# Kernel optimization log

Measured on AMD Instinct MI355X. Metric: run time of the kernel, lower is better.

## Reference

```python
import jax, jax.numpy as jnp
import numpy as np

B, S, LW = 64, 128, 20
CHAR_V, CHAR_E, CHAR_C = 100, 30, 30
WORD_V, WORD_E = 100000, 300
H, NC = 256, 25
F = WORD_E + CHAR_C  # 330


def setup_inputs() -> dict:
    key = jax.random.key(0)
    ks = jax.random.split(key, 16)
    u = lambda k, shape, s: jax.random.uniform(k, shape, jnp.float32, -s, s)
    sent = jax.random.randint(ks[0], (B, S), 0, WORD_V)
    word = jax.random.randint(ks[1], (B, S, LW), 0, CHAR_V)
    tag = jax.random.randint(ks[2], (B, S), 0, NC)
    lengths = jax.random.randint(ks[3], (B,), S // 2, S + 1)
    mask = jnp.arange(S)[None, :] < lengths[:, None]  # [B,S] bool, mask[:,0] all True

    word_table = u(ks[4], (WORD_V, WORD_E), 0.5)
    char_table = u(ks[5], (CHAR_V, CHAR_E), (3.0 / CHAR_E) ** 0.5)
    conv_w = u(ks[6], (CHAR_C, CHAR_E, 3), (6.0 / (CHAR_E * 3 + CHAR_C)) ** 0.5)
    conv_b = jnp.zeros((CHAR_C,), jnp.float32)

    def lstm_params(k):
        k1, k2 = jax.random.split(k)
        s_ih = (6.0 / (4 * H + F)) ** 0.5
        s_hh = (6.0 / (4 * H + H)) ** 0.5
        w_ih = u(k1, (4 * H, F), s_ih)
        w_hh = u(k2, (4 * H, H), s_hh)
        # b_ih + b_hh, each with forget-gate slice [H:2H] = 1.0 -> combined 2.0
        b = jnp.zeros((4 * H,), jnp.float32).at[H:2 * H].set(2.0)
        return w_ih, w_hh, b

    w_ih_f, w_hh_f, b_f = lstm_params(ks[7])
    w_ih_r, w_hh_r, b_r = lstm_params(ks[8])
    s_lin = (6.0 / (NC + 2 * H)) ** 0.5
    lin_w = u(ks[9], (NC, 2 * H), s_lin)
    lin_b = jnp.zeros((NC,), jnp.float32)
    start_t = u(ks[10], (NC,), 0.1)
    end_t = u(ks[11], (NC,), 0.1)
    trans = u(ks[12], (NC, NC), 0.1)
    return dict(word_table=word_table, char_table=char_table, conv_w=conv_w,
                conv_b=conv_b, w_ih_f=w_ih_f, w_hh_f=w_hh_f, b_f=b_f,
                w_ih_r=w_ih_r, w_hh_r=w_hh_r, b_r=b_r, lin_w=lin_w, lin_b=lin_b,
                start_t=start_t, end_t=end_t, trans=trans,
                sent=sent, word=word, tag=tag, mask=mask)


def _lstm_dir(x, w_ih, w_hh, b, reverse):
    # x: [B,S,F] -> precompute input projections time-major [S,B,4H]
    gx = jnp.einsum('bsf,gf->sbg', x, w_ih) + b
    bsz = x.shape[0]
    hs = w_hh.shape[1]

    def step(carry, g):
        h, c = carry
        g = g + h @ w_hh.T
        i, f, gg, o = jnp.split(g, 4, axis=-1)
        c = jax.nn.sigmoid(f) * c + jax.nn.sigmoid(i) * jnp.tanh(gg)
        h = jax.nn.sigmoid(o) * jnp.tanh(c)
        return (h, c), h

    init = (jnp.zeros((bsz, hs), x.dtype), jnp.zeros((bsz, hs), x.dtype))
    _, hseq = jax.lax.scan(step, init, gx, reverse=reverse)
    return hseq  # [S,B,H]


def _crf_nll(em, tg, mk, start_t, end_t, trans):
    # em: [S,B,C] emissions; tg: [S,B] int; mk: [S,B] float (mk[0]=1)
    bsz = em.shape[1]
    bidx = jnp.arange(bsz)
    # numerator: gold path score
    em_tag = jnp.take_along_axis(em, tg[..., None], axis=-1)[..., 0]   # [S,B]
    tr = trans[tg[:-1], tg[1:]]                                        # [S-1,B]
    score = start_t[tg[0]] + em_tag[0] + jnp.sum(mk[1:] * (tr + em_tag[1:]), axis=0)
    last = mk.sum(0).astype(jnp.int32) - 1
    score = score + end_t[tg[last, bidx]]
    # denominator: forward algorithm (logsumexp scan over time)
    alpha0 = start_t[None, :] + em[0]                                   # [B,C]

    def step(alpha, xs):
        em_t, mk_t = xs
        nxt = jax.nn.logsumexp(alpha[:, :, None] + trans[None, :, :] + em_t[:, None, :], axis=1)
        alpha = jnp.where(mk_t[:, None] > 0, nxt, alpha)
        return alpha, None

    alpha, _ = jax.lax.scan(step, alpha0, (em[1:], mk[1:]))
    logZ = jax.nn.logsumexp(alpha + end_t[None, :], axis=1)
    return -jnp.sum(score - logZ)  # model returns -log_likelihood (reduction='sum')


def reference(word_table, char_table, conv_w, conv_b, w_ih_f, w_hh_f, b_f,
              w_ih_r, w_hh_r, b_r, lin_w, lin_b, start_t, end_t, trans,
              sent, word, tag, mask):
    # --- char CNN encoder (dropout = identity in eval; no ReLU in original forward) ---
    ct = char_table.at[0].set(0.0)                      # padding_idx=0
    cemb = ct[word]                                     # [B,S,LW,E]
    x = cemb.reshape(B * S, LW, CHAR_E).transpose(0, 2, 1)  # [BS,E,LW]
    conv = jax.lax.conv_general_dilated(
        x, conv_w, window_strides=(1,), padding=[(1, 1)],
        dimension_numbers=('NCH', 'OIH', 'NCH')) + conv_b[None, :, None]
    char_feat = conv.max(axis=2).reshape(B, S, CHAR_C)  # global max-pool over chars
    # --- word embedding + concat ---
    wemb = word_table[sent]                             # [B,S,WORD_E]
    feat = jnp.concatenate([wemb, char_feat], axis=2)   # [B,S,F]
    # --- biLSTM ---
    hf = _lstm_dir(feat, w_ih_f, w_hh_f, b_f, reverse=False)
    hr = _lstm_dir(feat, w_ih_r, w_hh_r, b_r, reverse=True)
    h = jnp.concatenate([hf, hr], axis=-1)              # [S,B,2H] time-major
    em = h @ lin_w.T + lin_b                            # [S,B,NC]
    # --- CRF negative log-likelihood ---
    tg = tag.T
    mk = mask.T.astype(em.dtype)
    return _crf_nll(em, tg, mk, start_t, end_t, trans)
```

## Files before the change

### kernel.cpp

```cpp
#include <hip/hip_runtime.h>
#include <math.h>

#define B_  64
#define S_  128
#define LW_ 20
#define CHAR_E_ 30
#define CHAR_C_ 30
#define WORD_E_ 300
#define H_  256
#define NC_ 25
#define F_  330
#define KP_ 352
#define G4_ 1024
#define NG_ 2048

typedef __attribute__((ext_vector_type(8))) short short8;
typedef __attribute__((ext_vector_type(4))) float floatx4;
typedef __attribute__((ext_vector_type(8))) int int8v;

__device__ __forceinline__ unsigned int f2bf(float f){
    unsigned int u = __float_as_uint(f);
    u += 0x7FFFu + ((u>>16)&1u);
    return (u>>16) & 0xFFFFu;
}
__device__ __forceinline__ float bf2f(unsigned int v){ return __uint_as_float(v<<16); }

__device__ __forceinline__ float bfh(uint2 pk, int g){
    unsigned int w = (g < 2) ? pk.x : pk.y;
    return __uint_as_float((g & 1) ? (w & 0xffff0000u) : (w << 16));
}

__device__ __forceinline__ float sigf_(float x){ return __builtin_amdgcn_rcpf(1.0f+__expf(-x)); }
__device__ __forceinline__ float tanhf2_(float x){ return 1.0f - 2.0f*__builtin_amdgcn_rcpf(1.0f+__expf(2.0f*x)); }

__device__ __forceinline__ void gload16(const void* g, void* l){
    __builtin_amdgcn_global_load_lds((const __attribute__((address_space(1))) unsigned int*)g,
                                     (__attribute__((address_space(3))) unsigned int*)l, 16, 0, 0);
}

#define BAR_LDS() __asm__ volatile("s_waitcnt lgkmcnt(0)\n\ts_barrier" ::: "memory")

__global__ __launch_bounds__(256) void k_prep(const float* ct, const int* word,
        const float* cw, const float* cb, const float* wt, const int* sent,
        const float* wf, const float* wr, float* out,
        unsigned short* feat, unsigned short* wpack){
    __shared__ __align__(16) float x[8][32][20];
    int blk = blockIdx.x;
    int tid = threadIdx.x;
    if(blk < 1024){
        int tok0 = blk*8;
        for(int e = tid; e < 8*32*20; e += 256){
            int t  = e % 20;
            int ic = (e/20) & 31;
            int tl = e / 640;
            int id = word[(size_t)(tok0+tl)*LW_ + t];
            float v = 0.f;
            if(ic < CHAR_E_ && id != 0) v = ct[(size_t)id*CHAR_E_ + ic];
            x[tl][ic][t] = v;
        }
        __syncthreads();
        if(tid < 240){
            int tl = tid/30, oc = tid%30;
            float acc[22];
            #pragma unroll
            for(int q=0;q<22;q++) acc[q] = 0.f;
            for(int ic=0; ic<CHAR_E_; ic++){
                float w0 = cw[(oc*CHAR_E_+ic)*3+0];
                float w1 = cw[(oc*CHAR_E_+ic)*3+1];
                float w2 = cw[(oc*CHAR_E_+ic)*3+2];
                const float* xr = &x[tl][ic][0];
                #pragma unroll
                for(int t4=0;t4<5;t4++){
                    float4 v = ((const float4*)xr)[t4];
                    int t0 = t4*4;
                    acc[t0+2] += v.x*w0; acc[t0+1] += v.x*w1; acc[t0+0] += v.x*w2;
                    acc[t0+3] += v.y*w0; acc[t0+2] += v.y*w1; acc[t0+1] += v.y*w2;
                    acc[t0+4] += v.z*w0; acc[t0+3] += v.z*w1; acc[t0+2] += v.z*w2;
                    acc[t0+5] += v.w*w0; acc[t0+4] += v.w*w1; acc[t0+3] += v.w*w2;
                }
            }
            float m = -1e30f;
            #pragma unroll
            for(int t=0;t<20;t++){ float v = acc[t+1]; m = fmaxf(m, v); }
            m += cb[oc];
            feat[(size_t)(tok0+tl)*KP_ + WORD_E_ + oc] = (unsigned short)f2bf(m);
        }
    } else if(blk < 1024+2432){
        int idx = (blk-1024)*256 + tid;
        int n = idx / 76, e4 = idx % 76;
        if(e4 < 75){
            float4 v = ((const float4*)(wt + (size_t)sent[n]*WORD_E_))[e4];
            unsigned int lo = f2bf(v.x) | (f2bf(v.y)<<16);
            unsigned int hi = f2bf(v.z) | (f2bf(v.w)<<16);
            uint2 pr; pr.x = lo; pr.y = hi;
            *(uint2*)(feat + (size_t)n*KP_ + e4*4) = pr;
        } else {
            unsigned int* z = (unsigned int*)(feat + (size_t)n*KP_ + 330);
            #pragma unroll
            for(int q=0;q<11;q++) z[q] = 0;
        }
    } else if(blk < 6272){
        int i = (blk-3456)*256 + tid;
        int r = i / KP_, k = i % KP_;
        const float* src = (r < G4_) ? wf : wr;
        int rr = r & (G4_-1);
        wpack[i] = (k < F_) ? (unsigned short)f2bf(src[(size_t)rr*F_ + k]) : 0;
    } else {
        if(tid == 0) *out = 0.f;
    }
}

__global__ __launch_bounds__(256) void k_gemm(const unsigned short* A, const unsigned short* Bw,
                                              const float* bf, const float* br, unsigned short* gxb){
    __shared__ __align__(16) unsigned short As[128*32];
    __shared__ __align__(16) unsigned short Bs[128*32];
    int m0 = blockIdx.x*128, n0 = blockIdx.y*128;
    int tid = threadIdx.x;
    int w = tid>>6, lane = tid&63, q = lane>>4, l16 = lane&15;
    int wr = w>>1, wc = w&1;
    int srow0 = w*32 + (lane>>2);
    int scol  = (lane&3)*8;
    floatx4 acc[4][4];
    #pragma unroll
    for(int i=0;i<4;i++)
        #pragma unroll
        for(int j=0;j<4;j++) acc[i][j] = (floatx4){0.f,0.f,0.f,0.f};

    for(int k0=0; k0<KP_; k0+=32){
        __syncthreads();
        gload16(A  + (size_t)(m0+srow0   )*KP_ + k0 + scol, (unsigned short*)As + w*1024      );
        gload16(A  + (size_t)(m0+srow0+16)*KP_ + k0 + scol, (unsigned short*)As + w*1024 + 512);
        gload16(Bw + (size_t)(n0+srow0   )*KP_ + k0 + scol, (unsigned short*)Bs + w*1024      );
        gload16(Bw + (size_t)(n0+srow0+16)*KP_ + k0 + scol, (unsigned short*)Bs + w*1024 + 512);
        __asm__ volatile("s_waitcnt vmcnt(0)" ::: "memory");
        __syncthreads();
        short8 a_[4], b_[4];
        #pragma unroll
        for(int i=0;i<4;i++) a_[i] = *(const short8*)&As[(wr*64 + i*16 + l16)*32 + q*8];
        #pragma unroll
        for(int j=0;j<4;j++) b_[j] = *(const short8*)&Bs[(wc*64 + j*16 + l16)*32 + q*8];
        #pragma unroll
        for(int i=0;i<4;i++)
            #pragma unroll
            for(int j=0;j<4;j++)
                acc[i][j] = __builtin_amdgcn_mfma_f32_16x16x32_bf16(a_[i], b_[j], acc[i][j], 0,0,0);
    }
    #pragma unroll
    for(int j=0;j<4;j++){
        int n = n0 + wc*64 + j*16 + l16;
        int dirr = n >> 10, grow = n & 1023;
        float bias = dirr ? br[grow] : bf[grow];
        int gg = grow >> 8;
        int u  = grow & 255;
        int w8 = u >> 5, uu = u & 31;
        #pragma unroll
        for(int i=0;i<4;i++){
            int mb = m0 + wr*64 + i*16 + q*4;
            #pragma unroll
            for(int r=0;r<4;r++){
                int m = mb + r;
                int b = m >> 7, s = m & 127;
                size_t idx = ((size_t)(dirr*128 + s)*32 + (size_t)(b>>1))*2048
                           + (size_t)w8*256 + (size_t)((b&1)*32 + uu)*4 + gg;
                gxb[idx] = (unsigned short)f2bf(acc[i][j][r] + bias);
            }
        }
    }
}

__device__ __forceinline__ void lstm_step2(
    const unsigned char* hbb, unsigned char* hpub,
    float* wl, const int8v (*wreg)[2][2],
    int l16, int q, int bb, int uu,
    uint2 gg, float& cc, float* hs_ptr, const float inv_sc)
{
    floatx4 a[4][2];
    #pragma unroll
    for(int g=0; g<4; g++){
        a[g][0] = (floatx4){0.f,0.f,0.f,0.f};
        a[g][1] = (floatx4){0.f,0.f,0.f,0.f};
    }
    #pragma unroll
    for(int ki=0; ki<2; ki++){
        int8v hb = *(const int8v*)&hbb[l16*272 + ki*128 + q*32];
        #pragma unroll
        for(int g=0; g<4; g++){
            a[g][0] = __builtin_amdgcn_mfma_scale_f32_16x16x128_f8f6f4(wreg[g][0][ki], hb, a[g][0], 0,0,0,0x7F,0,0x7F);
            a[g][1] = __builtin_amdgcn_mfma_scale_f32_16x16x128_f8f6f4(wreg[g][1][ki], hb, a[g][1], 0,0,0,0x7F,0,0x7F);
        }
    }
    if(l16 < 2){
        #pragma unroll
        for(int g=0; g<4; g++){
            *(floatx4*)&wl[g*72 + l16*36 + q*4     ] = a[g][0];
            *(floatx4*)&wl[g*72 + l16*36 + q*4 + 16] = a[g][1];
        }
    }
    float iv = wl[0*72 + bb*36 + uu]*inv_sc + bfh(gg,0);
    float fv = wl[1*72 + bb*36 + uu]*inv_sc + bfh(gg,1);
    float gv = wl[2*72 + bb*36 + uu]*inv_sc + bfh(gg,2);
    float ov = wl[3*72 + bb*36 + uu]*inv_sc + bfh(gg,3);
    float cn = sigf_(fv)*cc + sigf_(iv)*tanhf2_(gv);
    cc = cn;
    float hv = sigf_(ov)*tanhf2_(cn);
    *hs_ptr = hv;
    unsigned int d8 = __builtin_amdgcn_cvt_pk_fp8_f32(hv*16.f, hv*16.f, 0u, false) & 0xFFu;
    unsigned int pk = d8
        | ((unsigned int)__shfl_down((int)d8, 1) << 8)
        | ((unsigned int)__shfl_down((int)d8, 2) << 16)
        | ((unsigned int)__shfl_down((int)d8, 3) << 24);
    if((uu & 3) == 0) *(unsigned int*)hpub = pk;
    BAR_LDS();
}

__global__ __launch_bounds__(512,2) void k_lstm_all(const float* whhf, const float* whhr,
        const unsigned short* gxb, float* hseq)
{
    int bid = blockIdx.x;
    int dir = bid >> 5;
    int bgrp = bid & 31;
    int tid = threadIdx.x;
    int w    = tid >> 6;
    int lane = tid & 63;
    int q    = lane >> 4;
    int l16  = lane & 15;
    int bb   = lane >> 5;
    int uu   = lane & 31;

    __shared__ __align__(16) unsigned char hlds[2][16*272];
    __shared__ __align__(16) float wregion[8*288];

    const float* whh = dir ? whhr : whhf;

    int8v wreg[4][2][2];
    #pragma unroll
    for(int g=0; g<4; g++){
        #pragma unroll
        for(int j=0; j<2; j++){
            const float* rp = whh + (size_t)(g*H_ + w*32 + j*16 + l16)*H_;
            #pragma unroll
            for(int ki=0; ki<2; ki++){
                const float* p = rp + ki*128 + q*32;
                int8v acc;
                #pragma unroll
                for(int wd=0; wd<8; wd++){
                    unsigned int d = 0;
                    d = __builtin_amdgcn_cvt_pk_fp8_f32(p[wd*4+0]*64.f, p[wd*4+1]*64.f, d, false);
                    d = __builtin_amdgcn_cvt_pk_fp8_f32(p[wd*4+2]*64.f, p[wd*4+3]*64.f, d, true);
                    acc[wd] = (int)d;
                }
                wreg[g][j][ki] = acc;
            }
        }
    }

    for(int i = tid; i < 2*16*272/4; i += 512) ((unsigned int*)hlds)[i] = 0;
    __syncthreads();

    const float inv_sc = 1.0f/1024.f;
    float cc = 0.f;

    int s0 = dir ? (S_-1) : 0;
    long gstep = dir ? -65536 : 65536;
    const unsigned short* gp = gxb + (size_t)(dir*128 + s0)*65536 + (size_t)bgrp*2048 + w*256 + lane*4;
    long hstep = dir ? -(long)(B_*H_) : (long)(B_*H_);
    float* hp = hseq + (((size_t)dir*S_ + s0)*B_ + bgrp*2 + bb)*H_ + w*32 + uu;

    float* wl = &wregion[w*288];
    unsigned char* hpw0 = &hlds[0][bb*272 + w*32 + (uu & ~3)];
    unsigned char* hpw1 = &hlds[1][bb*272 + w*32 + (uu & ~3)];

    uint2 P = *(const uint2*)gp; gp += gstep;
    uint2 Q;

    for(int t=0; t<S_; t+=2){
        Q = *(const uint2*)gp; gp += gstep;
        lstm_step2(&hlds[0][0], hpw1, wl, wreg, l16, q, bb, uu, P, cc, hp, inv_sc);
        hp += hstep;
        P = *(const uint2*)gp; gp += gstep;
        lstm_step2(&hlds[1][0], hpw0, wl, wreg, l16, q, bb, uu, Q, cc, hp, inv_sc);
        hp += hstep;
    }
}

__global__ __launch_bounds__(256) void k_em(const float* hseq, const float* lw, const float* lb, float* em){
    __shared__ __align__(16) float hb[8][516];
    int sb0 = blockIdx.x*8;
    int tid = threadIdx.x;
    for(int i = tid; i < 1024; i += 256){
        int p = i >> 7, r = i & 127;
        int sb = sb0 + p, s = sb >> 6, b = sb & 63;
        const float* src = (r < 64) ? (hseq + (((size_t)0*S_+s)*B_+b)*H_ + r*4)
                                    : (hseq + (((size_t)1*S_+s)*B_+b)*H_ + (r-64)*4);
        *(float4*)&hb[p][r*4] = *(const float4*)src;
    }
    __syncthreads();
    if(tid < 200){
        int p = tid / 25, nc = tid % 25;
        const float4* wv = (const float4*)(lw + (size_t)nc*2*H_);
        const float4* hv = (const float4*)&hb[p][0];
        float acc = lb[nc];
        #pragma unroll 16
        for(int k=0;k<128;k++){ float4 a=hv[k], ww=wv[k]; acc += a.x*ww.x + a.y*ww.y + a.z*ww.z + a.w*ww.w; }
        em[(size_t)(sb0+p)*NC_ + nc] = acc;
    }
}

__global__ void k_crf(const float* em, const int* tag, const void* mask,
                      const float* st, const float* et, const float* tr, float* out){
    __shared__ float trs[NC_*NC_];
    int b = blockIdx.x, tid = threadIdx.x;
    for(int i=tid;i<NC_*NC_;i+=64) trs[i]=tr[i];
    unsigned int first = *(const unsigned int*)mask;
    int ml;
    if(first == 1u) ml = 0;
    else if(first == 0x3F800000u) ml = 2;
    else ml = 1;
    __syncthreads();

    float part = 0.f; int cnt = 0;
    for(int s = tid; s < S_; s += 64){
        float mkv;
        {
            int off = b*S_ + s;
            if(ml==0)      mkv = ((const int*)mask)[off] ? 1.f : 0.f;
            else if(ml==1) mkv = ((const unsigned char*)mask)[off] ? 1.f : 0.f;
            else           mkv = ((const float*)mask)[off];
        }
        cnt += (mkv != 0.f) ? 1 : 0;
        if(s == 0){
            int t0 = tag[b*S_];
            part += st[t0] + em[((size_t)0*B_ + b)*NC_ + t0];
        } else {
            int tp = tag[b*S_ + s-1], tc = tag[b*S_ + s];
            part += mkv * (trs[tp*NC_ + tc] + em[((size_t)s*B_ + b)*NC_ + tc]);
        }
    }
    for(int o=32;o>0;o>>=1){ part += __shfl_down(part, o); cnt += __shfl_down(cnt, o); }
    float score = 0.f;
    int len = __shfl(cnt, 0);
    float score0 = __shfl(part, 0);
    if(tid == 0) score = score0 + et[ tag[b*S_ + len-1] ];

    float Ecol[NC_];
    if(tid < NC_){
        #pragma unroll
        for(int i=0;i<NC_;i++) Ecol[i] = __expf(trs[i*NC_+tid]);
    } else {
        #pragma unroll
        for(int i=0;i<NC_;i++) Ecol[i] = 0.f;
    }

    float alpha = (tid < NC_) ? (st[tid] + em[((size_t)0*B_ + b)*NC_ + tid]) : -1e30f;
    float em_n = (tid < NC_) ? em[((size_t)1*B_ + b)*NC_ + tid] : 0.f;

    for(int s=1;s<S_;s++){
        float em_c = em_n;
        if(s+1 < S_) em_n = (tid < NC_) ? em[((size_t)(s+1)*B_ + b)*NC_ + tid] : 0.f;
        float mkv;
        {
            int off = b*S_ + s;
            if(ml==0)      mkv = ((const int*)mask)[off] ? 1.f : 0.f;
            else if(ml==1) mkv = ((const unsigned char*)mask)[off] ? 1.f : 0.f;
            else           mkv = ((const float*)mask)[off];
        }
        float v = alpha;
        #pragma unroll
        for(int o=16;o>0;o>>=1) v = fmaxf(v, __shfl_down(v, o));
        float m = __shfl(v, 0);
        float a = (tid < NC_) ? __expf(alpha - m) : 0.f;
        float S0 = 0.f, S1 = 0.f;
        #pragma unroll
        for(int i=0;i<24;i+=2){ S0 += __shfl(a, i) * Ecol[i]; S1 += __shfl(a, i+1) * Ecol[i+1]; }
        S0 += __shfl(a, 24) * Ecol[24];
        float nxt = m + __logf(S0 + S1) + em_c;
        if(tid < NC_ && mkv != 0.f) alpha = nxt;
    }

    float v = (tid < NC_) ? (alpha + et[tid]) : -1e30f;
    float m2 = v;
    #pragma unroll
    for(int o=16;o>0;o>>=1) m2 = fmaxf(m2, __shfl_down(m2, o));
    m2 = __shfl(m2, 0);
    float e = (tid < NC_) ? __expf(v - m2) : 0.f;
    #pragma unroll
    for(int o=16;o>0;o>>=1) e += __shfl_down(e, o);
    if(tid == 0){
        float logZ = m2 + __logf(e);
        atomicAdd(out, logZ - score);
    }
}

extern "C" void kernel_launch(void* const* d_in, const int* in_sizes, int n_in,
                              void* d_out, int out_size, void* d_ws, size_t ws_size,
                              hipStream_t stream) {
    const float* word_table = (const float*)d_in[0];
    const float* char_table = (const float*)d_in[1];
    const float* conv_w     = (const float*)d_in[2];
    const float* conv_b     = (const float*)d_in[3];
    const float* w_ih_f     = (const float*)d_in[4];
    const float* w_hh_f     = (const float*)d_in[5];
    const float* b_f        = (const float*)d_in[6];
    const float* w_ih_r     = (const float*)d_in[7];
    const float* w_hh_r     = (const float*)d_in[8];
    const float* b_r        = (const float*)d_in[9];
    const float* lin_w      = (const float*)d_in[10];
    const float* lin_b      = (const float*)d_in[11];
    const float* start_t    = (const float*)d_in[12];
    const float* end_t      = (const float*)d_in[13];
    const float* trans      = (const float*)d_in[14];
    const int*   sent       = (const int*)d_in[15];
    const int*   word       = (const int*)d_in[16];
    const int*   tag        = (const int*)d_in[17];
    const void*  mask       = d_in[18];
    float* out = (float*)d_out;

    char* ws = (char*)d_ws;
    unsigned short* feat  = (unsigned short*)ws;
    unsigned short* wpack = (unsigned short*)(ws + 5767168);
    unsigned short* gxb   = (unsigned short*)(ws + 5767168 + 1441792);
    float* hseq = (float*)(ws + 5767168 + 1441792 + 33554432);
    float* em   = (float*)(ws + 5767168 + 1441792 + 33554432 + 16777216);

    k_prep<<<dim3(6273), 256, 0, stream>>>(char_table, word, conv_w, conv_b,
                                           word_table, sent, w_ih_f, w_ih_r, out, feat, wpack);
    k_gemm<<<dim3(B_*S_/128, NG_/128), 256, 0, stream>>>(feat, wpack, b_f, b_r, gxb);
    k_lstm_all<<<dim3(64), 512, 0, stream>>>(w_hh_f, w_hh_r, gxb, hseq);
    k_em<<<dim3(S_*B_/8), 256, 0, stream>>>(hseq, lin_w, lin_b, em);
    k_crf<<<dim3(B_), 64, 0, stream>>>(em, tag, mask, start_t, end_t, trans, out);
}
```

Before: 580.6 us.

## Split LSTM recurrence across 16 wavefronts of 16 hidden units each

The recurrent LSTM kernel now runs 1024 threads per block, with 16 wavefronts each owning 16 hidden units instead of 8 wavefronts owning 32. Each wave issues half as many MFMAs per step and stores the fp8 hidden byte directly, with no shuffle packing. The GEMM output layout for the gate pre-activations is changed to match the new per-wave slicing. The aim is a shorter serial per-step critical path. In exchange, only half the lanes do the elementwise gate math, and the per-step barrier now covers more waves.

```diff
diff --git a/kernel.cpp b/kernel.cpp
--- a/kernel.cpp
+++ b/kernel.cpp
@@ -150,9 +150,10 @@
         int n = n0 + wc*64 + j*16 + l16;
         int dirr = n >> 10, grow = n & 1023;
         float bias = dirr ? br[grow] : bf[grow];
-        int gg = grow >> 8;
-        int u  = grow & 255;
-        int w8 = u >> 5, uu = u & 31;
+        int gg  = grow >> 8;
+        int ug  = grow & 255;
+        int w16 = ug >> 4, u = ug & 15;
+        int ubase = w16*128 + u*4 + gg;
         #pragma unroll
         for(int i=0;i<4;i++){
             int mb = m0 + wr*64 + i*16 + q*4;
@@ -160,125 +161,113 @@
             for(int r=0;r<4;r++){
                 int m = mb + r;
                 int b = m >> 7, s = m & 127;
-                size_t idx = ((size_t)(dirr*128 + s)*32 + (size_t)(b>>1))*2048
-                           + (size_t)w8*256 + (size_t)((b&1)*32 + uu)*4 + gg;
+                size_t idx = ((size_t)((dirr*128 + s)*32 + (b>>1)))*2048
+                           + (size_t)(ubase + (b&1)*64);
                 gxb[idx] = (unsigned short)f2bf(acc[i][j][r] + bias);
             }
         }
     }
 }
 
-__device__ __forceinline__ void lstm_step2(
+__device__ __forceinline__ void lstm_step16w(
     const unsigned char* hbb, unsigned char* hpub,
-    float* wl, const int8v (*wreg)[2][2],
-    int l16, int q, int bb, int uu,
+    float* wl, const int8v (*wreg)[2],
+    int l16, int q, int lane,
     uint2 gg, float& cc, float* hs_ptr, const float inv_sc)
 {
-    floatx4 a[4][2];
-    #pragma unroll
-    for(int g=0; g<4; g++){
-        a[g][0] = (floatx4){0.f,0.f,0.f,0.f};
-        a[g][1] = (floatx4){0.f,0.f,0.f,0.f};
-    }
+    floatx4 a[4];
+    #pragma unroll
+    for(int g=0; g<4; g++) a[g] = (floatx4){0.f,0.f,0.f,0.f};
     #pragma unroll
     for(int ki=0; ki<2; ki++){
         int8v hb = *(const int8v*)&hbb[l16*272 + ki*128 + q*32];
         #pragma unroll
-        for(int g=0; g<4; g++){
-            a[g][0] = __builtin_amdgcn_mfma_scale_f32_16x16x128_f8f6f4(wreg[g][0][ki], hb, a[g][0], 0,0,0,0x7F,0,0x7F);
-            a[g][1] = __builtin_amdgcn_mfma_scale_f32_16x16x128_f8f6f4(wreg[g][1][ki], hb, a[g][1], 0,0,0,0x7F,0,0x7F);
-        }
+        for(int g=0; g<4; g++)
+            a[g] = __builtin_amdgcn_mfma_scale_f32_16x16x128_f8f6f4(wreg[g][ki], hb, a[g], 0,0,0,0x7F,0,0x7F);
     }
     if(l16 < 2){
         #pragma unroll
-        for(int g=0; g<4; g++){
-            *(floatx4*)&wl[g*72 + l16*36 + q*4     ] = a[g][0];
-            *(floatx4*)&wl[g*72 + l16*36 + q*4 + 16] = a[g][1];
-        }
-    }
-    float iv = wl[0*72 + bb*36 + uu]*inv_sc + bfh(gg,0);
-    float fv = wl[1*72 + bb*36 + uu]*inv_sc + bfh(gg,1);
-    float gv = wl[2*72 + bb*36 + uu]*inv_sc + bfh(gg,2);
-    float ov = wl[3*72 + bb*36 + uu]*inv_sc + bfh(gg,3);
-    float cn = sigf_(fv)*cc + sigf_(iv)*tanhf2_(gv);
-    cc = cn;
-    float hv = sigf_(ov)*tanhf2_(cn);
-    *hs_ptr = hv;
-    unsigned int d8 = __builtin_amdgcn_cvt_pk_fp8_f32(hv*16.f, hv*16.f, 0u, false) & 0xFFu;
-    unsigned int pk = d8
-        | ((unsigned int)__shfl_down((int)d8, 1) << 8)
-        | ((unsigned int)__shfl_down((int)d8, 2) << 16)
-        | ((unsigned int)__shfl_down((int)d8, 3) << 24);
-    if((uu & 3) == 0) *(unsigned int*)hpub = pk;
+        for(int g=0; g<4; g++)
+            *(floatx4*)&wl[g*32 + l16*16 + q*4] = a[g];
+    }
+    if(lane < 32){
+        float iv = wl[0*32 + lane]*inv_sc + bfh(gg,0);
+        float fv = wl[1*32 + lane]*inv_sc + bfh(gg,1);
+        float gv = wl[2*32 + lane]*inv_sc + bfh(gg,2);
+        float ov = wl[3*32 + lane]*inv_sc + bfh(gg,3);
+        float cn = sigf_(fv)*cc + sigf_(iv)*tanhf2_(gv);
+        cc = cn;
+        float hv = sigf_(ov)*tanhf2_(cn);
+        *hs_ptr = hv;
+        unsigned int d8 = __builtin_amdgcn_cvt_pk_fp8_f32(hv*16.f, hv*16.f, 0u, false) & 0xFFu;
+        *hpub = (unsigned char)d8;
+    }
     BAR_LDS();
 }
 
-__global__ __launch_bounds__(512,2) void k_lstm_all(const float* whhf, const float* whhr,
+__global__ __launch_bounds__(1024,4) void k_lstm_all(const float* whhf, const float* whhr,
         const unsigned short* gxb, float* hseq)
 {
     int bid = blockIdx.x;
     int dir = bid >> 5;
     int bgrp = bid & 31;
     int tid = threadIdx.x;
-    int w    = tid >> 6;
+    int w16  = tid >> 6;
     int lane = tid & 63;
     int q    = lane >> 4;
     int l16  = lane & 15;
-    int bb   = lane >> 5;
-    int uu   = lane & 31;
+    int bb   = lane >> 4;
+    int u    = lane & 15;
 
     __shared__ __align__(16) unsigned char hlds[2][16*272];
-    __shared__ __align__(16) float wregion[8*288];
+    __shared__ __align__(16) float wregion[16*128];
 
     const float* whh = dir ? whhr : whhf;
 
-    int8v wreg[4][2][2];
+    int8v wreg[4][2];
     #pragma unroll
     for(int g=0; g<4; g++){
-        #pragma unroll
-        for(int j=0; j<2; j++){
-            const float* rp = whh + (size_t)(g*H_ + w*32 + j*16 + l16)*H_;
-            #pragma unroll
-            for(int ki=0; ki<2; ki++){
-                const float* p = rp + ki*128 + q*32;
-                int8v acc;
-                #pragma unroll
-                for(int wd=0; wd<8; wd++){
-                    unsigned int d = 0;
-                    d = __builtin_amdgcn_cvt_pk_fp8_f32(p[wd*4+0]*64.f, p[wd*4+1]*64.f, d, false);
-                    d = __builtin_amdgcn_cvt_pk_fp8_f32(p[wd*4+2]*64.f, p[wd*4+3]*64.f, d, true);
-                    acc[wd] = (int)d;
-                }
-                wreg[g][j][ki] = acc;
+        const float* rp = whh + (size_t)(g*H_ + w16*16 + l16)*H_;
+        #pragma unroll
+        for(int ki=0; ki<2; ki++){
+            const float* p = rp + ki*128 + q*32;
+            int8v acc;
+            #pragma unroll
+            for(int wd=0; wd<8; wd++){
+                unsigned int d = 0;
+                d = __builtin_amdgcn_cvt_pk_fp8_f32(p[wd*4+0]*64.f, p[wd*4+1]*64.f, d, false);
+                d = __builtin_amdgcn_cvt_pk_fp8_f32(p[wd*4+2]*64.f, p[wd*4+3]*64.f, d, true);
+                acc[wd] = (int)d;
             }
-        }
-    }
-
-    for(int i = tid; i < 2*16*272/4; i += 512) ((unsigned int*)hlds)[i] = 0;
+            wreg[g][ki] = acc;
+        }
+    }
+
+    for(int i = tid; i < 2*16*272/4; i += 1024) ((unsigned int*)hlds)[i] = 0;
     __syncthreads();
 
     const float inv_sc = 1.0f/1024.f;
     float cc = 0.f;
 
     int s0 = dir ? (S_-1) : 0;
-    long gstep = dir ? -65536 : 65536;
-    const unsigned short* gp = gxb + (size_t)(dir*128 + s0)*65536 + (size_t)bgrp*2048 + w*256 + lane*4;
+    long gstep = dir ? -65536L : 65536L;
+    const unsigned short* gp = gxb + ((size_t)((dir*128 + s0)*32 + bgrp))*2048 + w16*128 + lane*4;
     long hstep = dir ? -(long)(B_*H_) : (long)(B_*H_);
-    float* hp = hseq + (((size_t)dir*S_ + s0)*B_ + bgrp*2 + bb)*H_ + w*32 + uu;
-
-    float* wl = &wregion[w*288];
-    unsigned char* hpw0 = &hlds[0][bb*272 + w*32 + (uu & ~3)];
-    unsigned char* hpw1 = &hlds[1][bb*272 + w*32 + (uu & ~3)];
+    float* hp = hseq + (((size_t)dir*S_ + s0)*B_ + bgrp*2 + bb)*H_ + w16*16 + u;
+
+    float* wl = &wregion[w16*128];
+    unsigned char* hpw0 = &hlds[0][bb*272 + w16*16 + u];
+    unsigned char* hpw1 = &hlds[1][bb*272 + w16*16 + u];
 
     uint2 P = *(const uint2*)gp; gp += gstep;
     uint2 Q;
 
     for(int t=0; t<S_; t+=2){
         Q = *(const uint2*)gp; gp += gstep;
-        lstm_step2(&hlds[0][0], hpw1, wl, wreg, l16, q, bb, uu, P, cc, hp, inv_sc);
+        lstm_step16w(&hlds[0][0], hpw1, wl, wreg, l16, q, lane, P, cc, hp, inv_sc);
         hp += hstep;
         P = *(const uint2*)gp; gp += gstep;
-        lstm_step2(&hlds[1][0], hpw0, wl, wreg, l16, q, bb, uu, Q, cc, hp, inv_sc);
+        lstm_step16w(&hlds[1][0], hpw0, wl, wreg, l16, q, lane, Q, cc, hp, inv_sc);
         hp += hstep;
     }
 }
@@ -425,7 +414,7 @@
     k_prep<<<dim3(6273), 256, 0, stream>>>(char_table, word, conv_w, conv_b,
                                            word_table, sent, w_ih_f, w_ih_r, out, feat, wpack);
     k_gemm<<<dim3(B_*S_/128, NG_/128), 256, 0, stream>>>(feat, wpack, b_f, b_r, gxb);
-    k_lstm_all<<<dim3(64), 512, 0, stream>>>(w_hh_f, w_hh_r, gxb, hseq);
+    k_lstm_all<<<dim3(64), 1024, 0, stream>>>(w_hh_f, w_hh_r, gxb, hseq);
     k_em<<<dim3(S_*B_/8), 256, 0, stream>>>(hseq, lin_w, lin_b, em);
     k_crf<<<dim3(B_), 64, 0, stream>>>(em, tag, mask, start_t, end_t, trans, out);
 }
```

After: 571.7 us, median of 2. About the same (-1.5%).
